# Kernel tuning notes

Hardware: AMD Instinct MI355X
Metric: run time of the kernel (lower is better)

## Reference

```python
import jax, jax.numpy as jnp
import numpy as np

N = 8192      # number of samples (x.shape[0])
D = 64        # out_feat / spectral embedding dim
K_NN = 32     # config['school']['k']
KP1 = 64      # columns in idx (>= K_NN + 1)
N_PROJ_ITERS = 100  # Newton iterations for simplex projection


def setup_inputs() -> dict:
    key = jax.random.key(0)
    k1, k2, k3, k4 = jax.random.split(key, 4)
    Y = jax.random.normal(k1, (N, D), jnp.float32)
    semantic_H = jax.random.normal(k2, (N, D), jnp.float32)
    ortho_H = jax.random.normal(k3, (N, D), jnp.float32)
    idx = jax.random.randint(k4, (N, KP1), 0, N)
    return {"Y": Y, "semantic_H": semantic_H, "ortho_H": ortho_H,
            "idx": idx, "alpha": 1, "beta": 1}


def eproj_simplex_rows(v, k=1.0):
    """Project each row of v onto the simplex {x >= 0, sum(x) = k}.
    Fixed-iteration Newton solve for the Lagrange multiplier (matches the
    iterative EProjSimplex_new_matrix; it is a fixed point once converged)."""
    n = v.shape[1]
    v0 = v - v.mean(axis=1, keepdims=True) + k / n   # shift so sum(v0) = k per row

    def body(_, lam):
        v1 = v0 - lam[:, None]
        pos = v1 > 0
        npos = jnp.maximum(pos.sum(axis=1), 1)       # -g
        f = jnp.where(pos, v1, 0.0).sum(axis=1) - k  # constraint residual
        return lam + f / npos                         # lam - f/g

    lam = jax.lax.fori_loop(0, N_PROJ_ITERS, body,
                            jnp.zeros(v.shape[0], v.dtype))
    return jnp.maximum(v0 - lam[:, None], 0.0)


def reference(Y, semantic_H, ortho_H, idx, alpha, beta):
    num = Y.shape[0]
    idxa0 = idx[:, 1:K_NN + 1]                                   # [N, k]
    # kNN gather + pairwise L2 distances (O(N*k*d), no dense NxN distances)
    dfi = jnp.sqrt(((Y[:, None, :] - Y[idxa0]) ** 2).sum(-1) + 1e-8)          # [N, k]
    dxi = jnp.sqrt(((ortho_H[:, None, :] - ortho_H[idxa0]) ** 2).sum(-1) + 1e-8)
    ad = -(dxi + beta * dfi) / (2 * alpha)
    w = eproj_simplex_rows(ad)                                   # [N, k] simplex weights
    # scatter into dense NxN adjacency (faithful to A.scatter_(1, idxa0, w))
    rows = jnp.arange(num)[:, None]
    A = jnp.zeros((num, num), Y.dtype).at[rows, idxa0].set(w)
    embs_hom = A @ semantic_H                                    # [N, D]
    return embs_hom, A, Y
```

## Files before the change

### kernel.cpp

```cpp
#include <hip/hip_runtime.h>

#define NROWS 8192
#define DDIM  64
#define KNN   32
#define MAXIT 100

__device__ __forceinline__ float scalar_val(const void* p) {
    int iv = *(const int*)p;
    if (iv > -1000000 && iv < 1000000) return (float)iv;
    return *(const float*)p;
}

__global__ __launch_bounds__(256, 4) void school_fused_kernel(
    const float* __restrict__ Y,
    const float* __restrict__ semH,
    const float* __restrict__ orthoH,
    const int*   __restrict__ idx,
    const void*  alpha_p,
    const void*  beta_p,
    float* __restrict__ embs,
    float* __restrict__ A,
    float* __restrict__ Yout)
{
    __shared__ int    col_s[8][KNN];
    __shared__ float  ad_s[8][KNN];
    __shared__ float2 cw_s[8][KNN];

    const int tid  = threadIdx.x;
    const int j    = tid & 31;
    const int r    = tid >> 5;
    const int row0 = blockIdx.x * 8;
    const int row  = row0 + r;

    const float alpha = scalar_val(alpha_p);
    const float beta  = scalar_val(beta_p);

    const int col = idx[row * 64 + 1 + j];
    col_s[r][j] = col;

    const float4* Y4 = (const float4*)Y;
    const float4* O4 = (const float4*)orthoH;
    const int p = j & 3;
    const int Q = j >> 2;
    const int hbase = tid & 32;

    const int c0 = __shfl(col, hbase | (0 * 8 + Q), 64);
    const int c1 = __shfl(col, hbase | (1 * 8 + Q), 64);
    const int c2 = __shfl(col, hbase | (2 * 8 + Q), 64);
    const int c3 = __shfl(col, hbase | (3 * 8 + Q), 64);

    float4 oy0 = Y4[(size_t)row * 16 + p +  0];
    float4 oy1 = Y4[(size_t)row * 16 + p +  4];
    float4 oy2 = Y4[(size_t)row * 16 + p +  8];
    float4 oy3 = Y4[(size_t)row * 16 + p + 12];
    float4 oo0 = O4[(size_t)row * 16 + p +  0];
    float4 oo1 = O4[(size_t)row * 16 + p +  4];
    float4 oo2 = O4[(size_t)row * 16 + p +  8];
    float4 oo3 = O4[(size_t)row * 16 + p + 12];

    const int cq[4] = {c0, c1, c2, c3};
    #pragma unroll
    for (int b = 0; b < 4; ++b) {
        const int cidx = b * 8 + Q;
        const int c = cq[b];
        float dY = 0.f, dO = 0.f;
        #define ACC_PH(ph, oy, oo)                                          \
        {                                                                   \
            float4 gY = Y4[(size_t)c * 16 + p + 4 * ph];                    \
            float4 gO = O4[(size_t)c * 16 + p + 4 * ph];                    \
            float ex = oy.x - gY.x, ey = oy.y - gY.y,                       \
                  ez = oy.z - gY.z, ew = oy.w - gY.w;                       \
            dY += ex * ex + ey * ey + ez * ez + ew * ew;                    \
            ex = oo.x - gO.x; ey = oo.y - gO.y;                             \
            ez = oo.z - gO.z; ew = oo.w - gO.w;                             \
            dO += ex * ex + ey * ey + ez * ez + ew * ew;                    \
        }
        ACC_PH(0, oy0, oo0)
        ACC_PH(1, oy1, oo1)
        ACC_PH(2, oy2, oo2)
        ACC_PH(3, oy3, oo3)
        #undef ACC_PH
        dY += __shfl_xor(dY, 1, 64);
        dY += __shfl_xor(dY, 2, 64);
        dO += __shfl_xor(dO, 1, 64);
        dO += __shfl_xor(dO, 2, 64);
        if (p == 0) {
            float dfv = sqrtf(dY + 1e-8f);
            float dxv = sqrtf(dO + 1e-8f);
            ad_s[r][cidx] = -(dxv + beta * dfv) / (2.f * alpha);
        }
    }
    const float ad = ad_s[r][j];

    float s = ad;
    #pragma unroll
    for (int mm = 1; mm <= 16; mm <<= 1) s += __shfl_xor(s, mm, 64);
    const float v0 = ad - s * (1.f / 32.f) + (1.f / 32.f);

    const unsigned long long halfsh = (unsigned long long)(tid & 32);
    const unsigned long long halfmask = 0xFFFFFFFFull << halfsh;
    float lam = 0.f;
    #pragma unroll 1
    for (int it = 0; it < MAXIT; ++it) {
        float v1 = v0 - lam;
        bool pos = v1 > 0.f;
        float pp = pos ? v1 : 0.f;
        #pragma unroll
        for (int mm = 1; mm <= 16; mm <<= 1) pp += __shfl_xor(pp, mm, 64);
        float c = (float)__popcll(__ballot(pos ? 1 : 0) & halfmask);
        float step = (pp - 1.f) / fmaxf(c, 1.f);
        lam += step;
        if (__all(fabsf(step) <= 1e-6f ? 1 : 0)) break;
    }
    const float w = fmaxf(v0 - lam, 0.f);

    cw_s[r][j] = make_float2(__int_as_float(col), w);

    const int myowner = (col >> 2) & 31;
    unsigned mymask = 0u;
    #pragma unroll
    for (int o = 0; o < 32; ++o) {
        unsigned long long b = __ballot(myowner == o ? 1 : 0);
        if (j == o) mymask = (unsigned)(b >> halfsh);
    }

    unsigned k0 = ~0u, k1 = ~0u, k2 = ~0u, k3 = ~0u;
    float f0 = 0.f, f1 = 0.f, f2 = 0.f, f3 = 0.f;
    int j0 = 0, j1 = 0, j2 = 0, j3 = 0;
    int nhit = 0;
    unsigned ovmask = 0u;
    {
        unsigned mrem = mymask;
        while (mrem) {
            int jj = __ffs(mrem) - 1;
            mrem &= mrem - 1;
            float2 cw = cw_s[r][jj];
            int c = __float_as_int(cw.x);
            unsigned key = ((unsigned)(c >> 7) << 2) | (unsigned)(c & 3);
            float wv = cw.y;
            if      (nhit > 0 && key == k0) { cw_s[r][j0].y = 0.f; f0 = wv; j0 = jj; }
            else if (nhit > 1 && key == k1) { cw_s[r][j1].y = 0.f; f1 = wv; j1 = jj; }
            else if (nhit > 2 && key == k2) { cw_s[r][j2].y = 0.f; f2 = wv; j2 = jj; }
            else if (nhit > 3 && key == k3) { cw_s[r][j3].y = 0.f; f3 = wv; j3 = jj; }
            else if (nhit == 0) { k0 = key; f0 = wv; j0 = jj; nhit = 1; }
            else if (nhit == 1) { k1 = key; f1 = wv; j1 = jj; nhit = 2; }
            else if (nhit == 2) { k2 = key; f2 = wv; j2 = jj; nhit = 3; }
            else if (nhit == 3) { k3 = key; f3 = wv; j3 = jj; nhit = 4; }
            else { ovmask |= 1u << jj; }
        }
    }

    {
        unsigned long long ovb = __ballot(ovmask != 0u ? 1 : 0);
        if (((ovb >> halfsh) & 0xFFFFFFFFull) != 0ull) {
            bool dead = false;
            for (int jj2 = j + 1; jj2 < 32; ++jj2)
                dead |= (col_s[r][jj2] == col);
            cw_s[r][j] = make_float2(__int_as_float(col), dead ? 0.f : w);
        }
    }

    {
        float2 acc = make_float2(0.f, 0.f);
        const float2* H2 = (const float2*)semH;
        #pragma unroll
        for (int jj = 0; jj < KNN; ++jj) {
            float2 cw = cw_s[r][jj];
            int   c   = __float_as_int(cw.x);
            float wv  = cw.y;
            float2 h = H2[(size_t)c * 32 + j];
            acc.x += wv * h.x;
            acc.y += wv * h.y;
        }
        ((float2*)embs)[(size_t)row * 32 + j] = acc;
    }

    {
        const float2* Y2 = (const float2*)(Y + (size_t)row0 * DDIM);
        float2* O2 = (float2*)(Yout + (size_t)row0 * DDIM);
        O2[tid] = Y2[tid];
    }

    {
        float4* Arow4 = (float4*)(A + (size_t)row * NROWS);
        #pragma unroll 4
        for (int ss = 0; ss < 64; ++ss) {
            float4 v = make_float4(0.f, 0.f, 0.f, 0.f);
            #define APPLY_SLOT(kk, ff)                                   \
                if ((kk >> 2) == (unsigned)ss) {                         \
                    int p_ = (int)(kk & 3u);                             \
                    v.x = (p_ == 0) ? ff : v.x;                          \
                    v.y = (p_ == 1) ? ff : v.y;                          \
                    v.z = (p_ == 2) ? ff : v.z;                          \
                    v.w = (p_ == 3) ? ff : v.w;                          \
                }
            APPLY_SLOT(k0, f0)
            APPLY_SLOT(k1, f1)
            APPLY_SLOT(k2, f2)
            APPLY_SLOT(k3, f3)
            #undef APPLY_SLOT
            Arow4[(ss << 5) + j] = v;
        }
    }

    if (ovmask) {
        asm volatile("s_waitcnt vmcnt(0)" ::: "memory");
        unsigned m = ovmask;
        while (m) {
            int jj = __ffs(m) - 1;
            m &= m - 1;
            int c = col_s[r][jj];
            A[(size_t)row * NROWS + c] = cw_s[r][jj].y;
            asm volatile("s_waitcnt vmcnt(0)" ::: "memory");
        }
    }
}

extern "C" void kernel_launch(void* const* d_in, const int* in_sizes, int n_in,
                              void* d_out, int out_size, void* d_ws, size_t ws_size,
                              hipStream_t stream) {
    const float* Y      = (const float*)d_in[0];
    const float* semH   = (const float*)d_in[1];
    const float* orthoH = (const float*)d_in[2];
    const int*   idx    = (const int*)d_in[3];
    const void*  alpha  = d_in[4];
    const void*  beta   = d_in[5];

    float* out  = (float*)d_out;
    float* embs = out;
    float* A    = out + (size_t)NROWS * DDIM;
    float* Yout = A + (size_t)NROWS * NROWS;

    school_fused_kernel<<<NROWS / 8, 256, 0, stream>>>(
        Y, semH, orthoH, idx, alpha, beta, embs, A, Yout);
}
```

Baseline: 56.73 us.

## Split dense A zero-fill into dedicated blocks and scatter weights in second kernel

Dedicates 256 extra blocks in the first kernel to a grid-stride zero-fill of the dense NxN adjacency, while the other blocks compute distances, simplex weights and embeddings. Instead of each row block writing its A row with in-register slot merging, the deduplicated (col, weight) pairs go to a workspace, and a second small kernel scatters them into A. This drops the per-row owner/slot bookkeeping and lets the large memset stream independently of the compute. The cost is an extra launch, a workspace round trip, and reliance on stream ordering so the scatter lands after the zero-fill.

```diff
diff --git a/kernel.cpp b/kernel.cpp
--- a/kernel.cpp
+++ b/kernel.cpp
@@ -4,6 +4,7 @@
 #define DDIM  64
 #define KNN   32
 #define MAXIT 100
+#define NFILL 256
 
 __device__ __forceinline__ float scalar_val(const void* p) {
     int iv = *(const int*)p;
@@ -11,7 +12,7 @@
     return *(const float*)p;
 }
 
-__global__ __launch_bounds__(256, 4) void school_fused_kernel(
+__global__ __launch_bounds__(256, 4) void school_d1_kernel(
     const float* __restrict__ Y,
     const float* __restrict__ semH,
     const float* __restrict__ orthoH,
@@ -20,16 +21,29 @@
     const void*  beta_p,
     float* __restrict__ embs,
     float* __restrict__ A,
-    float* __restrict__ Yout)
+    float* __restrict__ Yout,
+    float2* __restrict__ ws)
 {
+    const int tid = threadIdx.x;
+
+    if (blockIdx.x < NFILL) {
+        float4* A4 = (float4*)A;
+        const int total4 = NROWS * NROWS / 4;
+        const int stride = NFILL * 256;
+        const float4 z4 = make_float4(0.f, 0.f, 0.f, 0.f);
+        #pragma unroll 4
+        for (int i = blockIdx.x * 256 + tid; i < total4; i += stride)
+            A4[i] = z4;
+        return;
+    }
+
     __shared__ int    col_s[8][KNN];
     __shared__ float  ad_s[8][KNN];
     __shared__ float2 cw_s[8][KNN];
 
-    const int tid  = threadIdx.x;
     const int j    = tid & 31;
     const int r    = tid >> 5;
-    const int row0 = blockIdx.x * 8;
+    const int row0 = (blockIdx.x - NFILL) * 8;
     const int row  = row0 + r;
 
     const float alpha = scalar_val(alpha_p);
@@ -124,41 +138,53 @@
         if (j == o) mymask = (unsigned)(b >> halfsh);
     }
 
-    unsigned k0 = ~0u, k1 = ~0u, k2 = ~0u, k3 = ~0u;
-    float f0 = 0.f, f1 = 0.f, f2 = 0.f, f3 = 0.f;
-    int j0 = 0, j1 = 0, j2 = 0, j3 = 0;
+    int a0c = -1, a1c = -1, a2c = -1, a3c = -1;
+    int a0j = 0,  a1j = 0,  a2j = 0,  a3j = 0;
     int nhit = 0;
-    unsigned ovmask = 0u;
+    bool overflow = false;
     {
         unsigned mrem = mymask;
         while (mrem) {
             int jj = __ffs(mrem) - 1;
             mrem &= mrem - 1;
-            float2 cw = cw_s[r][jj];
-            int c = __float_as_int(cw.x);
-            unsigned key = ((unsigned)(c >> 7) << 2) | (unsigned)(c & 3);
-            float wv = cw.y;
-            if      (nhit > 0 && key == k0) { cw_s[r][j0].y = 0.f; f0 = wv; j0 = jj; }
-            else if (nhit > 1 && key == k1) { cw_s[r][j1].y = 0.f; f1 = wv; j1 = jj; }
-            else if (nhit > 2 && key == k2) { cw_s[r][j2].y = 0.f; f2 = wv; j2 = jj; }
-            else if (nhit > 3 && key == k3) { cw_s[r][j3].y = 0.f; f3 = wv; j3 = jj; }
-            else if (nhit == 0) { k0 = key; f0 = wv; j0 = jj; nhit = 1; }
-            else if (nhit == 1) { k1 = key; f1 = wv; j1 = jj; nhit = 2; }
-            else if (nhit == 2) { k2 = key; f2 = wv; j2 = jj; nhit = 3; }
-            else if (nhit == 3) { k3 = key; f3 = wv; j3 = jj; nhit = 4; }
-            else { ovmask |= 1u << jj; }
-        }
-    }
-
-    {
-        unsigned long long ovb = __ballot(ovmask != 0u ? 1 : 0);
+            int c = col_s[r][jj];
+            if      (nhit > 0 && c == a0c) {
+                cw_s[r][a0j] = make_float2(__int_as_float(c | 0x80000000), 0.f);
+                a0j = jj;
+            }
+            else if (nhit > 1 && c == a1c) {
+                cw_s[r][a1j] = make_float2(__int_as_float(c | 0x80000000), 0.f);
+                a1j = jj;
+            }
+            else if (nhit > 2 && c == a2c) {
+                cw_s[r][a2j] = make_float2(__int_as_float(c | 0x80000000), 0.f);
+                a2j = jj;
+            }
+            else if (nhit > 3 && c == a3c) {
+                cw_s[r][a3j] = make_float2(__int_as_float(c | 0x80000000), 0.f);
+                a3j = jj;
+            }
+            else if (nhit == 0) { a0c = c; a0j = jj; nhit = 1; }
+            else if (nhit == 1) { a1c = c; a1j = jj; nhit = 2; }
+            else if (nhit == 2) { a2c = c; a2j = jj; nhit = 3; }
+            else if (nhit == 3) { a3c = c; a3j = jj; nhit = 4; }
+            else { overflow = true; }
+        }
+    }
+
+    {
+        unsigned long long ovb = __ballot(overflow ? 1 : 0);
         if (((ovb >> halfsh) & 0xFFFFFFFFull) != 0ull) {
             bool dead = false;
             for (int jj2 = j + 1; jj2 < 32; ++jj2)
                 dead |= (col_s[r][jj2] == col);
-            cw_s[r][j] = make_float2(__int_as_float(col), dead ? 0.f : w);
-        }
-    }
+            cw_s[r][j] = make_float2(
+                __int_as_float(dead ? (col | 0x80000000) : col),
+                dead ? 0.f : w);
+        }
+    }
+
+    ws[(size_t)row * KNN + j] = cw_s[r][j];
 
     {
         float2 acc = make_float2(0.f, 0.f);
@@ -166,7 +192,7 @@
         #pragma unroll
         for (int jj = 0; jj < KNN; ++jj) {
             float2 cw = cw_s[r][jj];
-            int   c   = __float_as_int(cw.x);
+            int   c   = __float_as_int(cw.x) & 0x7FFFFFFF;
             float wv  = cw.y;
             float2 h = H2[(size_t)c * 32 + j];
             acc.x += wv * h.x;
@@ -180,40 +206,21 @@
         float2* O2 = (float2*)(Yout + (size_t)row0 * DDIM);
         O2[tid] = Y2[tid];
     }
-
-    {
-        float4* Arow4 = (float4*)(A + (size_t)row * NROWS);
-        #pragma unroll 4
-        for (int ss = 0; ss < 64; ++ss) {
-            float4 v = make_float4(0.f, 0.f, 0.f, 0.f);
-            #define APPLY_SLOT(kk, ff)                                   \
-                if ((kk >> 2) == (unsigned)ss) {                         \
-                    int p_ = (int)(kk & 3u);                             \
-                    v.x = (p_ == 0) ? ff : v.x;                          \
-                    v.y = (p_ == 1) ? ff : v.y;                          \
-                    v.z = (p_ == 2) ? ff : v.z;                          \
-                    v.w = (p_ == 3) ? ff : v.w;                          \
-                }
-            APPLY_SLOT(k0, f0)
-            APPLY_SLOT(k1, f1)
-            APPLY_SLOT(k2, f2)
-            APPLY_SLOT(k3, f3)
-            #undef APPLY_SLOT
-            Arow4[(ss << 5) + j] = v;
-        }
-    }
-
-    if (ovmask) {
-        asm volatile("s_waitcnt vmcnt(0)" ::: "memory");
-        unsigned m = ovmask;
-        while (m) {
-            int jj = __ffs(m) - 1;
-            m &= m - 1;
-            int c = col_s[r][jj];
-            A[(size_t)row * NROWS + c] = cw_s[r][jj].y;
-            asm volatile("s_waitcnt vmcnt(0)" ::: "memory");
-        }
-    }
+}
+
+__global__ __launch_bounds__(256, 8) void school_d2_kernel(
+    const float2* __restrict__ ws,
+    float* __restrict__ A)
+{
+    const int tid = threadIdx.x;
+    const int j   = tid & 31;
+    const int r   = tid >> 5;
+    const int row = blockIdx.x * 8 + r;
+
+    float2 cw = ws[(size_t)row * KNN + j];
+    int c = __float_as_int(cw.x);
+    if (c >= 0)
+        A[(size_t)row * NROWS + c] = cw.y;
 }
 
 extern "C" void kernel_launch(void* const* d_in, const int* in_sizes, int n_in,
@@ -231,6 +238,10 @@
     float* A    = out + (size_t)NROWS * DDIM;
     float* Yout = A + (size_t)NROWS * NROWS;
 
-    school_fused_kernel<<<NROWS / 8, 256, 0, stream>>>(
-        Y, semH, orthoH, idx, alpha, beta, embs, A, Yout);
-}
+    float2* ws = (float2*)d_ws;
+
+    school_d1_kernel<<<NFILL + NROWS / 8, 256, 0, stream>>>(
+        Y, semH, orthoH, idx, alpha, beta, embs, A, Yout, ws);
+
+    school_d2_kernel<<<NROWS / 8, 256, 0, stream>>>(ws, A);
+}
```

Result: slower. 58.60 us (+3.3%).

## Split dense A zero-fill into dedicated blocks interleaved with compute blocks

Applied to the files above, without the earlier changes.

Launches 1280 blocks in groups of five: one block in each group zero-fills the A row slots that no neighbour touches for 32 rows, and the other four do the distance, simplex projection, embedding and nonzero-slot writes for 8 rows each. The compute blocks now store only the float4 slots that contain neighbours. This separates the store-bound 256MB zero-fill from the latency-bound Newton loop so the two can overlap across CUs. It relies on the filler and compute blocks writing disjoint addresses and repeats the owner-mask computation in the filler blocks.

```diff
diff --git a/kernel.cpp b/kernel.cpp
--- a/kernel.cpp
+++ b/kernel.cpp
@@ -22,14 +22,64 @@
     float* __restrict__ A,
     float* __restrict__ Yout)
 {
+    const int tid   = threadIdx.x;
+    const int j     = tid & 31;
+    const int r     = tid >> 5;
+    const unsigned long long halfsh = (unsigned long long)(tid & 32);
+
+    if (blockIdx.x % 5 == 0) {
+        __shared__ int colf[4][8][32];
+        const int fb   = blockIdx.x / 5;
+        const int base = fb * 32;
+
+        int col4[4];
+        #pragma unroll
+        for (int pass = 0; pass < 4; ++pass) {
+            const int row = base + pass * 8 + r;
+            col4[pass] = idx[row * 64 + 1 + j];
+            colf[pass][r][j] = col4[pass];
+        }
+
+        unsigned long long hm[4];
+        #pragma unroll
+        for (int pass = 0; pass < 4; ++pass) {
+            const int myowner = (col4[pass] >> 2) & 31;
+            unsigned mymask = 0u;
+            #pragma unroll
+            for (int o = 0; o < 32; ++o) {
+                unsigned long long b = __ballot(myowner == o ? 1 : 0);
+                if (j == o) mymask = (unsigned)(b >> halfsh);
+            }
+            unsigned long long h = 0ull;
+            unsigned mrem = mymask;
+            while (mrem) {
+                int jj = __ffs(mrem) - 1;
+                mrem &= mrem - 1;
+                h |= 1ull << (colf[pass][r][jj] >> 7);
+            }
+            hm[pass] = h;
+        }
+
+        const float4 z4 = make_float4(0.f, 0.f, 0.f, 0.f);
+        #pragma unroll
+        for (int pass = 0; pass < 4; ++pass) {
+            float4* Arow4 = (float4*)(A + (size_t)(base + pass * 8 + r) * NROWS);
+            const unsigned long long h = hm[pass];
+            #pragma unroll 8
+            for (int ss = 0; ss < 64; ++ss) {
+                if (!((h >> ss) & 1ull))
+                    Arow4[(ss << 5) + j] = z4;
+            }
+        }
+        return;
+    }
+
     __shared__ int    col_s[8][KNN];
     __shared__ float  ad_s[8][KNN];
     __shared__ float2 cw_s[8][KNN];
 
-    const int tid  = threadIdx.x;
-    const int j    = tid & 31;
-    const int r    = tid >> 5;
-    const int row0 = blockIdx.x * 8;
+    const int cb   = blockIdx.x - blockIdx.x / 5 - 1;
+    const int row0 = cb * 8;
     const int row  = row0 + r;
 
     const float alpha = scalar_val(alpha_p);
@@ -97,7 +147,6 @@
     for (int mm = 1; mm <= 16; mm <<= 1) s += __shfl_xor(s, mm, 64);
     const float v0 = ad - s * (1.f / 32.f) + (1.f / 32.f);
 
-    const unsigned long long halfsh = (unsigned long long)(tid & 32);
     const unsigned long long halfmask = 0xFFFFFFFFull << halfsh;
     float lam = 0.f;
     #pragma unroll 1
@@ -124,6 +173,7 @@
         if (j == o) mymask = (unsigned)(b >> halfsh);
     }
 
+    unsigned long long hitmask = 0ull;
     unsigned k0 = ~0u, k1 = ~0u, k2 = ~0u, k3 = ~0u;
     float f0 = 0.f, f1 = 0.f, f2 = 0.f, f3 = 0.f;
     int j0 = 0, j1 = 0, j2 = 0, j3 = 0;
@@ -137,6 +187,7 @@
             float2 cw = cw_s[r][jj];
             int c = __float_as_int(cw.x);
             unsigned key = ((unsigned)(c >> 7) << 2) | (unsigned)(c & 3);
+            hitmask |= 1ull << (c >> 7);
             float wv = cw.y;
             if      (nhit > 0 && key == k0) { cw_s[r][j0].y = 0.f; f0 = wv; j0 = jj; }
             else if (nhit > 1 && key == k1) { cw_s[r][j1].y = 0.f; f1 = wv; j1 = jj; }
@@ -183,11 +234,13 @@
 
     {
         float4* Arow4 = (float4*)(A + (size_t)row * NROWS);
-        #pragma unroll 4
-        for (int ss = 0; ss < 64; ++ss) {
+        unsigned long long mrem = hitmask;
+        while (mrem) {
+            int ss = __ffsll(mrem) - 1;
+            mrem &= mrem - 1;
             float4 v = make_float4(0.f, 0.f, 0.f, 0.f);
             #define APPLY_SLOT(kk, ff)                                   \
-                if ((kk >> 2) == (unsigned)ss) {                         \
+                if ((int)(kk >> 2) == ss) {                              \
                     int p_ = (int)(kk & 3u);                             \
                     v.x = (p_ == 0) ? ff : v.x;                          \
                     v.y = (p_ == 1) ? ff : v.y;                          \
@@ -231,6 +284,6 @@
     float* A    = out + (size_t)NROWS * DDIM;
     float* Yout = A + (size_t)NROWS * NROWS;
 
-    school_fused_kernel<<<NROWS / 8, 256, 0, stream>>>(
+    school_fused_kernel<<<1280, 256, 0, stream>>>(
         Y, semH, orthoH, idx, alpha, beta, embs, A, Yout);
 }
```

After: 63.87 us. +12.6%, slower.
